# Performance work log

Measured on AMD Instinct MI355X. Metric: run time of the kernel, lower is better.

## Reference

```python
import jax, jax.numpy as jnp
import numpy as np

NUM_HEADS = 16


def setup_inputs() -> dict:
    key = jax.random.key(0)
    ks = jax.random.split(key, 6)
    B, S, D = 2, 2048, 1024
    hidden_states = jax.random.normal(ks[0], (B, S, D), dtype=jnp.float32)
    attention_mask = jnp.zeros((B, 1, 1, S), dtype=jnp.float32)  # additive mask
    # Linear weights stored as [in, out] (equivalent to torch weight.T)
    W_qkv = jax.random.normal(ks[1], (D, 3 * D), dtype=jnp.float32) * (1.0 / np.sqrt(D))
    b_qkv = jnp.zeros((3 * D,), dtype=jnp.float32)
    W_proj = jax.random.normal(ks[2], (D, D), dtype=jnp.float32) * (1.0 / np.sqrt(D))
    b_proj = jnp.zeros((D,), dtype=jnp.float32)
    return {
        "hidden_states": hidden_states,
        "attention_mask": attention_mask,
        "W_qkv": W_qkv,
        "b_qkv": b_qkv,
        "W_proj": W_proj,
        "b_proj": b_proj,
    }


def reference(hidden_states, attention_mask, W_qkv, b_qkv, W_proj, b_proj):
    B, S, D = hidden_states.shape
    H = NUM_HEADS
    hd = D // H
    scale = 1.0 / jnp.sqrt(jnp.asarray(hd, hidden_states.dtype))

    qkv = hidden_states @ W_qkv + b_qkv            # [B,S,3D]
    q, k, v = jnp.split(qkv, 3, axis=-1)
    # [B,S,D] -> [B,H,S,hd]
    split_heads = lambda t: t.reshape(B, S, H, hd).transpose(0, 2, 1, 3)
    q, k, v = split_heads(q), split_heads(k), split_heads(v)

    scores = jnp.einsum("bhqd,bhkd->bhqk", q, k) * scale + attention_mask
    attn = jax.nn.softmax(scores, axis=-1)
    ctx = jnp.einsum("bhqk,bhkd->bhqd", attn, v)   # [B,H,S,hd]
    ctx = ctx.transpose(0, 2, 1, 3).reshape(B, S, D)
    return ctx @ W_proj + b_proj
```

## Files before the change

kernel.cpp:

```cpp
#include <hip/hip_runtime.h>
#include <hip/hip_bf16.h>

typedef short short8 __attribute__((ext_vector_type(8)));
typedef float floatx4 __attribute__((ext_vector_type(4)));
typedef int intx4 __attribute__((ext_vector_type(4)));
typedef int intx2 __attribute__((ext_vector_type(2)));

#define S_LEN 2048
#define DMODEL 1024
#define NH 16
#define HD 64
#define BATCH 2

static __device__ __forceinline__ short f2bf(float x) {
    __hip_bfloat16 h = __float2bfloat16(x);
    return *(short*)&h;
}

static __device__ __forceinline__ unsigned pk2(float lo, float hi) {
    unsigned a = (unsigned)(unsigned short)f2bf(lo);
    unsigned b = (unsigned)(unsigned short)f2bf(hi);
    return a | (b << 16);
}

static __device__ __forceinline__ void async_ld16(const __hip_bfloat16* g, __hip_bfloat16* l) {
    __builtin_amdgcn_global_load_lds(
        (const __attribute__((address_space(1))) unsigned int*)g,
        (__attribute__((address_space(3))) unsigned int*)l, 16, 0, 0);
}

__global__ __launch_bounds__(256) void cvt_kernel(const float* __restrict__ X,
                                                  __hip_bfloat16* __restrict__ Y) {
    int i = (blockIdx.x * 256 + threadIdx.x) * 8;
    floatx4 f0 = *(const floatx4*)&X[i];
    floatx4 f1 = *(const floatx4*)&X[i + 4];
    short8 s;
    s[0] = f2bf(f0[0]); s[1] = f2bf(f0[1]); s[2] = f2bf(f0[2]); s[3] = f2bf(f0[3]);
    s[4] = f2bf(f1[0]); s[5] = f2bf(f1[1]); s[6] = f2bf(f1[2]); s[7] = f2bf(f1[3]);
    *(short8*)&Y[i] = s;
}

__global__ void transpose_kernel(const float* __restrict__ W,
                                 __hip_bfloat16* __restrict__ Wt, int K, int N) {
    __shared__ float tile[32][33];
    int n0 = blockIdx.x * 32, k0 = blockIdx.y * 32;
    int tx = threadIdx.x, ty = threadIdx.y;
#pragma unroll
    for (int i = 0; i < 32; i += 8)
        tile[ty + i][tx] = W[(size_t)(k0 + ty + i) * N + n0 + tx];
    __syncthreads();
#pragma unroll
    for (int i = 0; i < 32; i += 8)
        Wt[(size_t)(n0 + ty + i) * K + k0 + tx] = __float2bfloat16(tile[tx][ty + i]);
}

__global__ __launch_bounds__(256) void gemm128(
    const __hip_bfloat16* __restrict__ A, const __hip_bfloat16* __restrict__ Bt,
    const float* __restrict__ bias, float* __restrict__ Cf,
    __hip_bfloat16* __restrict__ Qp, __hip_bfloat16* __restrict__ Kp,
    __hip_bfloat16* __restrict__ Vt, int M, int N, int K, int mode) {
    __shared__ __align__(16) __hip_bfloat16 As[128 * 32];
    __shared__ __align__(16) __hip_bfloat16 Bs[128 * 32];
    const int m0 = blockIdx.y * 128, n0 = blockIdx.x * 128;
    const int t = threadIdx.x;
    const int wave = t >> 6, lane = t & 63;
    const int quad = lane >> 4, m16 = lane & 15;
    const int wm = (wave >> 1) * 64, wn = (wave & 1) * 64;
    const int srow = lane >> 2, scol = (lane & 3) * 8;

    floatx4 acc[4][4] = {};
    for (int k0 = 0; k0 < K; k0 += 32) {
#pragma unroll
        for (int i = 0; i < 2; i++) {
            const int rbase = wave * 32 + i * 16;
            async_ld16(&A[(size_t)(m0 + rbase + srow) * K + k0 + scol], &As[rbase * 32]);
            async_ld16(&Bt[(size_t)(n0 + rbase + srow) * K + k0 + scol], &Bs[rbase * 32]);
        }
        __syncthreads();
        short8 af[4], bfr[4];
#pragma unroll
        for (int i = 0; i < 4; i++)
            af[i] = *(const short8*)&As[(wm + i * 16 + m16) * 32 + quad * 8];
#pragma unroll
        for (int j = 0; j < 4; j++)
            bfr[j] = *(const short8*)&Bs[(wn + j * 16 + m16) * 32 + quad * 8];
#pragma unroll
        for (int i = 0; i < 4; i++)
#pragma unroll
            for (int j = 0; j < 4; j++)
                acc[i][j] = __builtin_amdgcn_mfma_f32_16x16x32_bf16(af[i], bfr[j], acc[i][j], 0, 0, 0);
        __syncthreads();
    }
    if (mode == 0) {
#pragma unroll
        for (int i = 0; i < 4; i++)
#pragma unroll
            for (int j = 0; j < 4; j++) {
                int col = n0 + wn + j * 16 + m16;
                float bv = bias[col];
#pragma unroll
                for (int r = 0; r < 4; r++) {
                    int row = m0 + wm + i * 16 + quad * 4 + r;
                    Cf[(size_t)row * N + col] = acc[i][j][r] + bv;
                }
            }
    } else if (n0 < 2 * DMODEL) {
#pragma unroll
        for (int i = 0; i < 4; i++)
#pragma unroll
            for (int j = 0; j < 4; j++) {
                int col = n0 + wn + j * 16 + m16;
                float bv = bias[col];
#pragma unroll
                for (int r = 0; r < 4; r++) {
                    int row = m0 + wm + i * 16 + quad * 4 + r;
                    __hip_bfloat16 hv = __float2bfloat16(acc[i][j][r] + bv);
                    int tt = col >> 10, rem = col & 1023;
                    int h = rem >> 6, d = rem & 63;
                    int b = row >> 11, s = row & 2047;
                    if (tt == 0) Qp[((size_t)(b * NH + h) * S_LEN + s) * HD + d] = hv;
                    else         Kp[((size_t)(b * NH + h) * S_LEN + s) * HD + d] = hv;
                }
            }
    } else {
        char* T = (char*)As;
        const int bq = m0 >> 11;
        const int s_base = m0 & 2047;
        for (int p = 0; p < 4; p++) {
            if (wave == p) {
#pragma unroll
                for (int j = 0; j < 4; j++) {
                    const int drow = j * 16 + m16;
                    const float bv = bias[n0 + wn + j * 16 + m16];
                    const int within = (quad & 1) * 4;
#pragma unroll
                    for (int i = 0; i < 4; i++) {
                        const int colc = i * 2 + (quad >> 1);
                        const int physc = colc ^ (drow & 7);
                        intx2 v;
                        v[0] = (int)pk2(acc[i][j][0] + bv, acc[i][j][1] + bv);
                        v[1] = (int)pk2(acc[i][j][2] + bv, acc[i][j][3] + bv);
                        *(intx2*)(T + drow * 128 + physc * 16 + within * 2) = v;
                    }
                }
            }
            __syncthreads();
            {
                const int dl = t >> 2;
                const int sseg = (t & 3) * 16;
                const int c0 = (sseg >> 3) ^ (dl & 7);
                const int c1 = ((sseg >> 3) + 1) ^ (dl & 7);
                short8 a0 = *(const short8*)(T + dl * 128 + c0 * 16);
                short8 a1 = *(const short8*)(T + dl * 128 + c1 * 16);
                const int hh = (n0 - 2 * DMODEL + (p & 1) * 64) >> 6;
                const int sg = s_base + (p >> 1) * 64 + sseg;
                __hip_bfloat16* dst = &Vt[((size_t)(bq * NH + hh) * HD + dl) * S_LEN + sg];
                *(short8*)dst = a0;
                *(short8*)(dst + 8) = a1;
            }
            __syncthreads();
        }
    }
}

__global__ __launch_bounds__(512, 8) void attn_kernel(
    const __hip_bfloat16* __restrict__ Q,
    const __hip_bfloat16* __restrict__ K,
    const __hip_bfloat16* __restrict__ Vt,
    const float* __restrict__ mask,
    __hip_bfloat16* __restrict__ ctx) {
    __shared__ __align__(16) __hip_bfloat16 smem[16384];
    __shared__ float wsm[S_LEN];
    const int bh = blockIdx.x;
    const int b = bh >> 4, h = bh & 15;
    const int t = threadIdx.x, wave = t >> 6, lane = t & 63;
    const int team = wave >> 2, tw = wave & 3;
    const int quad = lane >> 4, m16 = lane & 15;
    const int qbase = blockIdx.y * 64 + tw * 16;
    const int ko = team * (S_LEN / 2);
    const __hip_bfloat16* Qh = Q + (size_t)bh * S_LEN * HD;
    const __hip_bfloat16* Kh = K + (size_t)bh * S_LEN * HD;
    const __hip_bfloat16* Vh = Vt + (size_t)bh * HD * S_LEN;
    const float* mb = mask + (size_t)b * S_LEN;
    const float LOG2E = 1.44269504f;
    const float scale2 = 0.125f * LOG2E;
    const float M_FIX2 = 20.0f * LOG2E;

    __hip_bfloat16* Ksb = smem + team * 8192;
    __hip_bfloat16* Vsb = smem + team * 8192 + 4096;

    {
        floatx4 mv = *(const floatx4*)&mb[t * 4];
        floatx4 wv;
#pragma unroll
        for (int r = 0; r < 4; r++) wv[r] = __builtin_fmaf(mv[r], LOG2E, -M_FIX2);
        *(floatx4*)&wsm[t * 4] = wv;
    }

    const int kr = lane >> 3, kc = lane & 7;
    const int kgoff = (tw * 8 + kr) * HD + ((kc ^ kr) * 8);
    const int vr = lane >> 2, vc = lane & 3;
    const int vd = tw * 16 + vr;
    const int vgoff = vd * S_LEN + (((vc ^ ((vd >> 1) & 3))) * 8);
    __hip_bfloat16* kdst0 = Ksb + tw * 512;
    __hip_bfloat16* kdst1 = Ksb + 2048 + tw * 512;
    __hip_bfloat16* vdst0 = Vsb + tw * 512;
    __hip_bfloat16* vdst1 = Vsb + 2048 + tw * 512;

    short8 aq0 = *(const short8*)&Qh[(size_t)(qbase + m16) * HD + quad * 8];
    short8 aq1 = *(const short8*)&Qh[(size_t)(qbase + m16) * HD + 32 + quad * 8];

    const short ONEB = (short)0x3F80;
    const short8 ones = {ONEB, ONEB, ONEB, ONEB, ONEB, ONEB, ONEB, ONEB};

    async_ld16(&Kh[(size_t)ko * HD + kgoff], kdst0);
    async_ld16(&Vh[(size_t)ko + vgoff], vdst0);
    __syncthreads();

    floatx4 o[4] = {};
    floatx4 lacc = {};
    const int swk = m16 & 7;
    const int e = quad & 1;
    const int C = ((quad & 1) << 1) | (quad >> 1);
    const int vsl = (C ^ ((m16 >> 1) & 3)) * 8;

    const int NIT = (S_LEN / 2) / 32;
    for (int it = 0; it < NIT; it++) {
        const int k0 = it * 32;
        const int cur = it & 1;
        if (it < NIT - 1) {
            async_ld16(&Kh[(size_t)(ko + k0 + 32) * HD + kgoff], cur ? kdst0 : kdst1);
            async_ld16(&Vh[(size_t)(ko + k0 + 32) + vgoff], cur ? vdst0 : vdst1);
        }

        const __hip_bfloat16* Kc = Ksb + cur * 2048;
        floatx4 sc[2] = {};
        __builtin_amdgcn_s_setprio(1);
#pragma unroll
        for (int kt = 0; kt < 2; kt++) {
            const int row = kt * 16 + m16;
            short8 ak0 = *(const short8*)&Kc[row * 64 + ((quad ^ swk) * 8)];
            short8 ak1 = *(const short8*)&Kc[row * 64 + (((quad + 4) ^ swk) * 8)];
            sc[kt] = __builtin_amdgcn_mfma_f32_16x16x32_bf16(ak0, aq0, sc[kt], 0, 0, 0);
            sc[kt] = __builtin_amdgcn_mfma_f32_16x16x32_bf16(ak1, aq1, sc[kt], 0, 0, 0);
        }
        __builtin_amdgcn_s_setprio(0);

        unsigned dk[2][2];
#pragma unroll
        for (int kt = 0; kt < 2; kt++) {
            floatx4 wv = *(const floatx4*)&wsm[ko + k0 + kt * 16 + quad * 4];
            float p0 = __builtin_amdgcn_exp2f(__builtin_fmaf(sc[kt][0], scale2, wv[0]));
            float p1 = __builtin_amdgcn_exp2f(__builtin_fmaf(sc[kt][1], scale2, wv[1]));
            float p2 = __builtin_amdgcn_exp2f(__builtin_fmaf(sc[kt][2], scale2, wv[2]));
            float p3 = __builtin_amdgcn_exp2f(__builtin_fmaf(sc[kt][3], scale2, wv[3]));
            dk[kt][0] = pk2(p0, p1);
            dk[kt][1] = pk2(p2, p3);
        }

        unsigned s0 = e ? dk[0][0] : dk[1][0];
        unsigned s1 = e ? dk[0][1] : dk[1][1];
        unsigned r0 = (unsigned)__builtin_amdgcn_ds_swizzle((int)s0, 0x401F);
        unsigned r1 = (unsigned)__builtin_amdgcn_ds_swizzle((int)s1, 0x401F);
        intx4 wa;
        wa[0] = (int)(e ? r0 : dk[0][0]);
        wa[1] = (int)(e ? r1 : dk[0][1]);
        wa[2] = (int)(e ? dk[1][0] : r0);
        wa[3] = (int)(e ? dk[1][1] : r1);
        short8 ap = *(short8*)&wa;

        const __hip_bfloat16* Vc = Vsb + cur * 2048;
        __builtin_amdgcn_s_setprio(1);
        lacc = __builtin_amdgcn_mfma_f32_16x16x32_bf16(ap, ones, lacc, 0, 0, 0);
#pragma unroll
        for (int tt = 0; tt < 4; tt++) {
            const int d = tt * 16 + m16;
            short8 bv = *(const short8*)&Vc[d * 32 + vsl];
            o[tt] = __builtin_amdgcn_mfma_f32_16x16x32_bf16(ap, bv, o[tt], 0, 0, 0);
        }
        __builtin_amdgcn_s_setprio(0);
        __syncthreads();
    }

    float* xch = (float*)smem;
    const int xi = (tw * 64 + lane) * 21;
    if (team == 1) {
#pragma unroll
        for (int tt = 0; tt < 4; tt++)
#pragma unroll
            for (int r = 0; r < 4; r++) xch[xi + tt * 4 + r] = o[tt][r];
#pragma unroll
        for (int r = 0; r < 4; r++) xch[xi + 16 + r] = lacc[r];
    }
    __syncthreads();
    if (team == 0) {
        float li[4];
#pragma unroll
        for (int r = 0; r < 4; r++) li[r] = 1.0f / (lacc[r] + xch[xi + 16 + r]);
#pragma unroll
        for (int tt = 0; tt < 4; tt++)
#pragma unroll
            for (int r = 0; r < 4; r++) {
                int srow = qbase + quad * 4 + r;
                int d = tt * 16 + m16;
                float v = (o[tt][r] + xch[xi + tt * 4 + r]) * li[r];
                ctx[((size_t)b * S_LEN + srow) * DMODEL + h * HD + d] = __float2bfloat16(v);
            }
    }
}

extern "C" void kernel_launch(void* const* d_in, const int* in_sizes, int n_in,
                              void* d_out, int out_size, void* d_ws, size_t ws_size,
                              hipStream_t stream) {
    (void)in_sizes; (void)n_in; (void)out_size; (void)ws_size;
    const float* hidden = (const float*)d_in[0];
    const float* mask   = (const float*)d_in[1];
    const float* Wqkv   = (const float*)d_in[2];
    const float* bqkv   = (const float*)d_in[3];
    const float* Wproj  = (const float*)d_in[4];
    const float* bproj  = (const float*)d_in[5];
    float* out = (float*)d_out;

    __hip_bfloat16* ws = (__hip_bfloat16*)d_ws;
    const size_t Q4 = 4u * 1024 * 1024;
    __hip_bfloat16* Qp      = ws;
    __hip_bfloat16* Kp      = ws + 1 * Q4;
    __hip_bfloat16* Vt      = ws + 2 * Q4;
    __hip_bfloat16* hid_bf  = ws + 3 * Q4;
    __hip_bfloat16* ctx     = ws + 3 * Q4;
    __hip_bfloat16* Wqkv_t  = ws + 4 * Q4;
    __hip_bfloat16* Wproj_t = ws + 4 * Q4;

    cvt_kernel<<<dim3(4 * 1024 * 1024 / 2048), 256, 0, stream>>>(hidden, hid_bf);
    transpose_kernel<<<dim3(3072 / 32, 1024 / 32), dim3(32, 8), 0, stream>>>(Wqkv, Wqkv_t, 1024, 3072);

    gemm128<<<dim3(3072 / 128, 4096 / 128), 256, 0, stream>>>(
        hid_bf, Wqkv_t, bqkv, nullptr, Qp, Kp, Vt, BATCH * S_LEN, 3 * DMODEL, DMODEL, 1);

    transpose_kernel<<<dim3(1024 / 32, 1024 / 32), dim3(32, 8), 0, stream>>>(Wproj, Wproj_t, 1024, 1024);

    attn_kernel<<<dim3(BATCH * NH, S_LEN / 64), 512, 0, stream>>>(Qp, Kp, Vt, mask, ctx);

    gemm128<<<dim3(1024 / 128, 4096 / 128), 256, 0, stream>>>(
        ctx, Wproj_t, bproj, out, nullptr, nullptr, nullptr, BATCH * S_LEN, DMODEL, DMODEL, 0);
}
```

Before: 223.7 us.

## Double-buffer GEMM LDS tiles and remap blocks across XCDs

The bf16 MFMA GEMM now keeps two LDS buffers for the A and B tiles. It issues the async global-to-LDS loads for the next K-slice before computing on the current one, so the load latency can overlap the MFMA work. Global offsets are hoisted out of the K loop. Block indices are also permuted so consecutive blocks that share data land on the same XCD, aiming for better L2 reuse. This doubles LDS use per block, which may lower occupancy, and the remap assumes the grid size is divisible by 8.

```diff
diff --git a/kernel.cpp b/kernel.cpp
--- a/kernel.cpp
+++ b/kernel.cpp
@@ -59,31 +59,49 @@
     const float* __restrict__ bias, float* __restrict__ Cf,
     __hip_bfloat16* __restrict__ Qp, __hip_bfloat16* __restrict__ Kp,
     __hip_bfloat16* __restrict__ Vt, int M, int N, int K, int mode) {
-    __shared__ __align__(16) __hip_bfloat16 As[128 * 32];
-    __shared__ __align__(16) __hip_bfloat16 Bs[128 * 32];
-    const int m0 = blockIdx.y * 128, n0 = blockIdx.x * 128;
+    __shared__ __align__(16) __hip_bfloat16 As[2][128 * 32];
+    __shared__ __align__(16) __hip_bfloat16 Bs[2][128 * 32];
+    const int gx = gridDim.x, gy = gridDim.y;
+    const int flat = blockIdx.y * gx + blockIdx.x;
+    const int cpx = (gx * gy) >> 3;
+    const int id2 = (flat & 7) * cpx + (flat >> 3);
+    const int m0 = (id2 % gy) * 128, n0 = (id2 / gy) * 128;
     const int t = threadIdx.x;
     const int wave = t >> 6, lane = t & 63;
     const int quad = lane >> 4, m16 = lane & 15;
     const int wm = (wave >> 1) * 64, wn = (wave & 1) * 64;
     const int srow = lane >> 2, scol = (lane & 3) * 8;
 
+    const int rb0 = wave * 32, rb1 = wave * 32 + 16;
+    const size_t aoff0 = (size_t)(m0 + rb0 + srow) * K + scol;
+    const size_t aoff1 = (size_t)(m0 + rb1 + srow) * K + scol;
+    const size_t boff0 = (size_t)(n0 + rb0 + srow) * K + scol;
+    const size_t boff1 = (size_t)(n0 + rb1 + srow) * K + scol;
+
+    async_ld16(&A[aoff0], &As[0][rb0 * 32]);
+    async_ld16(&A[aoff1], &As[0][rb1 * 32]);
+    async_ld16(&Bt[boff0], &Bs[0][rb0 * 32]);
+    async_ld16(&Bt[boff1], &Bs[0][rb1 * 32]);
+    __syncthreads();
+
     floatx4 acc[4][4] = {};
-    for (int k0 = 0; k0 < K; k0 += 32) {
-#pragma unroll
-        for (int i = 0; i < 2; i++) {
-            const int rbase = wave * 32 + i * 16;
-            async_ld16(&A[(size_t)(m0 + rbase + srow) * K + k0 + scol], &As[rbase * 32]);
-            async_ld16(&Bt[(size_t)(n0 + rbase + srow) * K + k0 + scol], &Bs[rbase * 32]);
-        }
-        __syncthreads();
+    const int NI = K >> 5;
+    for (int it = 0; it < NI; ++it) {
+        const int cur = it & 1;
+        if (it < NI - 1) {
+            const int k0 = (it + 1) * 32;
+            async_ld16(&A[aoff0 + k0], &As[cur ^ 1][rb0 * 32]);
+            async_ld16(&A[aoff1 + k0], &As[cur ^ 1][rb1 * 32]);
+            async_ld16(&Bt[boff0 + k0], &Bs[cur ^ 1][rb0 * 32]);
+            async_ld16(&Bt[boff1 + k0], &Bs[cur ^ 1][rb1 * 32]);
+        }
         short8 af[4], bfr[4];
 #pragma unroll
         for (int i = 0; i < 4; i++)
-            af[i] = *(const short8*)&As[(wm + i * 16 + m16) * 32 + quad * 8];
+            af[i] = *(const short8*)&As[cur][(wm + i * 16 + m16) * 32 + quad * 8];
 #pragma unroll
         for (int j = 0; j < 4; j++)
-            bfr[j] = *(const short8*)&Bs[(wn + j * 16 + m16) * 32 + quad * 8];
+            bfr[j] = *(const short8*)&Bs[cur][(wn + j * 16 + m16) * 32 + quad * 8];
 #pragma unroll
         for (int i = 0; i < 4; i++)
 #pragma unroll
```

Measured after the change: 215.2 us. -3.8%, faster.
